# Kernel tuning notes

Hardware: AMD Instinct MI355X
Metric: run time of the kernel (lower is better)

Reference implementation:

```python
import jax, jax.numpy as jnp
import numpy as np

NUM_HEADS = 12
TOPK = 4


def setup_inputs() -> dict:
    key = jax.random.key(0)
    ks = jax.random.split(key, 5)
    B, N, C = 32, 577, 768
    s = 0.02
    return {
        "x": jax.random.normal(ks[0], (B, N, C), jnp.float32),
        "qkv_w": jax.random.normal(ks[1], (3 * C, C), jnp.float32) * s,
        "qkv_b": jax.random.normal(ks[2], (3 * C,), jnp.float32) * s,
        "proj_w": jax.random.normal(ks[3], (C, C), jnp.float32) * s,
        "proj_b": jax.random.normal(ks[4], (C,), jnp.float32) * s,
    }


def reference(x, qkv_w, qkv_b, proj_w, proj_b):
    B, N, C = x.shape
    H = NUM_HEADS
    D = C // H
    scale = D ** -0.5  # 0.125, matches original_attention.scale

    # qkv projection: (B,N,3C) -> (3,B,H,N,D)
    qkv = (x @ qkv_w.T + qkv_b).reshape(B, N, 3, H, D).transpose(2, 0, 3, 1, 4)
    q, k, v = qkv[0], qkv[1], qkv[2]

    # heuristic head routing: mean squared query energy per head
    scores = jnp.mean(q.astype(jnp.float32) ** 2, axis=(0, 2, 3))  # (H,)
    _, idx = jax.lax.top_k(scores, TOPK)
    idx = jnp.sort(idx)  # (topk,)

    q_sel = q[:, idx]  # (B,topk,N,D)
    k_sel = k[:, idx]
    v_sel = v[:, idx]

    attn = jax.nn.softmax(jnp.einsum('bhnd,bhmd->bhnm', q_sel, k_sel) * scale, axis=-1)
    y_sel = jnp.einsum('bhnm,bhmd->bhnd', attn, v_sel)  # (B,topk,N,D)

    # scatter selected heads back into full-size tensors (as in the torch module)
    y_full = jnp.zeros((B, H, N, D), x.dtype).at[:, idx].set(y_sel)
    x_out = y_full.transpose(0, 2, 1, 3).reshape(B, N, C) @ proj_w.T + proj_b

    attn_full = jnp.zeros((B, H, N, N), x.dtype).at[:, idx].set(attn)
    return x_out, attn_full
```

## Files before the change

kernel.cpp:

```cpp
#include <hip/hip_runtime.h>
#include <hip/hip_bf16.h>
#include <stdint.h>
#include <stddef.h>

#define B_ 32
#define N_ 577
#define C_ 768
#define H_ 12
#define D_ 64
#define M_ (B_*N_)
#define K3_ (3*C_)
#define NP_ 640
#define NN_ (N_*N_)

typedef __bf16 bf16x8_t __attribute__((ext_vector_type(8)));
typedef float f32x4 __attribute__((ext_vector_type(4)));
typedef unsigned short u16x8 __attribute__((ext_vector_type(8)));
typedef unsigned short u16x4 __attribute__((ext_vector_type(4)));

static __device__ __forceinline__ f32x4 mfma16(u16x8 a, u16x8 b, f32x4 c) {
  return __builtin_amdgcn_mfma_f32_16x16x32_bf16(
      __builtin_bit_cast(bf16x8_t, a), __builtin_bit_cast(bf16x8_t, b), c, 0, 0, 0);
}

static __device__ __forceinline__ unsigned short f2bf(float x) {
  unsigned int u = __builtin_bit_cast(unsigned int, x);
  u += 0x7fffu + ((u >> 16) & 1u);
  return (unsigned short)(u >> 16);
}

static __device__ __forceinline__ void glds16(const unsigned short* g, unsigned short* l) {
  __builtin_amdgcn_global_load_lds(
      (__attribute__((address_space(1))) void*)g,
      (__attribute__((address_space(3))) void*)l,
      16, 0, 0);
}

__global__ void k_cvt(const float* __restrict__ src, unsigned short* __restrict__ dst, int n4,
                      float* __restrict__ zeroptr) {
  if (zeroptr && blockIdx.x == 0 && threadIdx.x < 16) zeroptr[threadIdx.x] = 0.f;
  int stride = gridDim.x * blockDim.x;
  for (int i = blockIdx.x * blockDim.x + threadIdx.x; i < n4; i += stride) {
    float4 v = ((const float4*)src)[i];
    u16x4 o;
    o[0] = f2bf(v.x); o[1] = f2bf(v.y); o[2] = f2bf(v.z); o[3] = f2bf(v.w);
    *(u16x4*)(dst + (size_t)i * 4) = o;
  }
}

#define ZROWS_ 6
#define ZPER_ 146948
template<int MODE>
__global__ void k_gemm(const unsigned short* __restrict__ A,
                       const unsigned short* __restrict__ Bm,
                       const float* __restrict__ bias,
                       unsigned short* __restrict__ qb,
                       unsigned short* __restrict__ kb,
                       unsigned short* __restrict__ vb,
                       float* __restrict__ scores,
                       float* __restrict__ out,
                       int Mtot, int Ktot)
{
  __shared__ unsigned short As[128 * 32];
  __shared__ unsigned short Bs[128 * 32];
  const int tid = threadIdx.x;

  if (MODE == 0 && blockIdx.y < ZROWS_) {
    const int zblk = blockIdx.y * 145 + blockIdx.x;
    const size_t Z = (size_t)B_ * H_ * NN_;
    size_t s0 = (size_t)zblk * ZPER_;
    size_t len = ZPER_;
    if (s0 + len > Z) len = Z - s0;
    float* zo = out + s0;
    const float4 z4 = {0.f, 0.f, 0.f, 0.f};
    for (size_t t = tid * 4; t + 4 <= len; t += 4096)
      *(float4*)(zo + t) = z4;
    return;
  }

  const int bm = blockIdx.x;
  const int bn = (MODE == 0) ? (blockIdx.y - ZROWS_) : blockIdx.y;
  const int w = tid >> 6, l = tid & 63;
  const int wm = w >> 1, wn = w & 1;
  const int lr = l & 15, lg = l >> 4;
  const int lk = lg * 8;
  f32x4 acc[4][4] = {};
  const int rowA0 = bm * 128, rowB0 = bn * 128;
  const int le0 = w * 1024 + l * 8;
  const int kiters = Ktot >> 5;
  for (int kt = 0; kt < kiters; ++kt) {
    __syncthreads();
    #pragma unroll
    for (int c = 0; c < 2; ++c) {
      int lea = le0 + c * 512;
      int ra = lea >> 5, ka = lea & 31;
      glds16(A  + (size_t)(rowA0 + ra) * Ktot + kt * 32 + ka, As + (w * 2 + c) * 512);
      glds16(Bm + (size_t)(rowB0 + ra) * Ktot + kt * 32 + ka, Bs + (w * 2 + c) * 512);
    }
    __syncthreads();
    u16x8 af[4], bfr[4];
    #pragma unroll
    for (int i = 0; i < 4; ++i)
      af[i] = *(const u16x8*)(As + (wm * 64 + i * 16 + lr) * 32 + lk);
    #pragma unroll
    for (int j = 0; j < 4; ++j)
      bfr[j] = *(const u16x8*)(Bs + (wn * 64 + j * 16 + lr) * 32 + lk);
    #pragma unroll
    for (int i = 0; i < 4; ++i)
      #pragma unroll
      for (int j = 0; j < 4; ++j)
        acc[i][j] = mfma16(af[i], bfr[j], acc[i][j]);
  }

  const int rbase = lg * 4;
  if (MODE == 0) {
    const int n0 = rowB0 + wn * 64;
    const int t0 = n0 / C_;
    const int h0 = (n0 % C_) >> 6;
    unsigned short* dstbuf = (t0 == 0) ? qb : ((t0 == 1) ? kb : vb);
    float bs[4];
    #pragma unroll
    for (int j = 0; j < 4; ++j) bs[j] = bias[n0 + j * 16 + lr];
    float sq = 0.f;
    #pragma unroll
    for (int i = 0; i < 4; ++i) {
      const int mbase = rowA0 + wm * 64 + i * 16 + rbase;
      const int bb0 = mbase / N_;
      const int np0 = mbase - bb0 * N_;
      #pragma unroll
      for (int r = 0; r < 4; ++r) {
        const int mm = mbase + r;
        if (mm < Mtot) {
          int np = np0 + r, bb = bb0;
          if (np >= N_) { np -= N_; bb += 1; }
          unsigned short* drow = dstbuf + (((size_t)(bb * H_ + h0)) * N_ + np) * D_;
          #pragma unroll
          for (int j = 0; j < 4; ++j) {
            const float v = acc[i][j][r] + bs[j];
            if (t0 == 0) sq += v * v;
            drow[j * 16 + lr] = f2bf(v);
          }
        }
      }
    }
    if (t0 == 0) {
      #pragma unroll
      for (int s2 = 1; s2 < 64; s2 <<= 1) sq += __shfl_xor(sq, s2);
      if (l == 0) atomicAdd(scores + h0, sq);
    }
  } else {
    #pragma unroll
    for (int j = 0; j < 4; ++j) {
      const int n = rowB0 + wn * 64 + j * 16 + lr;
      const float bsj = bias[n];
      #pragma unroll
      for (int i = 0; i < 4; ++i) {
        const int mbase = rowA0 + wm * 64 + i * 16 + rbase;
        #pragma unroll
        for (int r = 0; r < 4; ++r) {
          const int mm = mbase + r;
          if (mm < Mtot) out[(size_t)mm * C_ + n] = acc[i][j][r] + bsj;
        }
      }
    }
  }
}

__global__ void k_topk(const float* __restrict__ scores, int* __restrict__ idxp) {
  if (threadIdx.x == 0 && blockIdx.x == 0) {
    float s[H_];
    bool used[H_];
    for (int i = 0; i < H_; ++i) { s[i] = scores[i]; used[i] = false; }
    int sel[4];
    for (int t = 0; t < 4; ++t) {
      int best = 0; float bv = -3.0e38f;
      for (int i = 0; i < H_; ++i)
        if (!used[i] && s[i] > bv) { bv = s[i]; best = i; }
      used[best] = true; sel[t] = best;
    }
    for (int a = 0; a < 4; ++a)
      for (int b = a + 1; b < 4; ++b)
        if (sel[b] < sel[a]) { int t = sel[a]; sel[a] = sel[b]; sel[b] = t; }
    for (int t = 0; t < 4; ++t) idxp[t] = sel[t];
  }
}

__global__ void k_gatherpw(const float* __restrict__ pw, const int* __restrict__ idxp,
                           unsigned short* __restrict__ pwsel) {
  int i = blockIdx.x * 256 + threadIdx.x;
  if (i >= C_ * 256) return;
  int c = i >> 8, j = i & 255;
  int h = idxp[j >> 6], d = j & 63;
  pwsel[i] = f2bf(pw[(size_t)c * C_ + h * 64 + d]);
}

__global__ void k_transv(const unsigned short* __restrict__ vb, unsigned short* __restrict__ vT,
                         const int* __restrict__ idxp) {
  __shared__ unsigned short t[64][72];
  const int bid = blockIdx.x;
  const int nt = bid % 10;
  const int p  = bid / 10;
  const int b  = p >> 2, hs = p & 3;
  const int h  = idxp[hs];
  const size_t bh_src = (size_t)(b * H_ + h);
  const size_t bh_dst = (size_t)(b * 4 + hs);
  const int n0 = nt * 64;
  const int tid = threadIdx.x;
  {
    const int r = tid >> 2, q4 = (tid & 3) * 16;
    const int n = n0 + r;
    u16x8 v0, v1;
    if (n < N_) {
      const unsigned short* src = vb + (bh_src * N_ + n) * D_ + q4;
      v0 = *(const u16x8*)(src);
      v1 = *(const u16x8*)(src + 8);
    } else {
      #pragma unroll
      for (int j = 0; j < 8; ++j) { v0[j] = 0; v1[j] = 0; }
    }
    *(u16x8*)&t[r][q4] = v0;
    *(u16x8*)&t[r][q4 + 8] = v1;
  }
  __syncthreads();
  {
    const int d = tid >> 2, nc = (tid & 3) * 16;
    u16x8 w0, w1;
    #pragma unroll
    for (int j = 0; j < 8; ++j) { w0[j] = t[nc + j][d]; w1[j] = t[nc + 8 + j][d]; }
    unsigned short* dst = vT + (bh_dst * D_ + d) * NP_ + n0 + nc;
    *(u16x8*)(dst) = w0;
    *(u16x8*)(dst + 8) = w1;
  }
}

__global__ void k_attn(const unsigned short* __restrict__ qb,
                       const unsigned short* __restrict__ kb,
                       const unsigned short* __restrict__ vT,
                       const int* __restrict__ idxp,
                       float* __restrict__ attn_out,
                       unsigned short* __restrict__ ysel)
{
  __shared__ unsigned short Plds[4][16][72];
  const int bid = blockIdx.x;

  const int qt = bid >> 7;
  const int pair = bid & 127;
  const int b  = pair >> 2;
  const int hs = pair & 3;
  const int h  = idxp[hs];
  const int tid = threadIdx.x;
  const int w = tid >> 6, l = tid & 63;
  const int lr = l & 15, lg = l >> 4, lk = lg * 8;
  const float sc2 = 0.125f * 1.44269504f;

  const size_t bh = (size_t)(b * H_ + h);
  const unsigned short* qbase = qb + bh * ((size_t)N_ * D_);
  const unsigned short* kbase = kb + bh * ((size_t)N_ * D_);
  const unsigned short* vbase = vT + (size_t)(b * 4 + hs) * ((size_t)D_ * NP_);
  float* aout = attn_out + bh * (size_t)NN_;

  const int qrow = qt * 64 + w * 16 + lr;
  const int qrc = (qrow < N_) ? qrow : (N_ - 1);
  u16x8 qf0 = *(const u16x8*)(qbase + (size_t)qrc * D_ + lk);
  u16x8 qf1 = *(const u16x8*)(qbase + (size_t)qrc * D_ + 32 + lk);

  float m2[4], lsum[4];
  #pragma unroll
  for (int r = 0; r < 4; ++r) { m2[r] = -1.0e30f; lsum[r] = 0.f; }

  for (int kt = 0; kt < 10; ++kt) {
    f32x4 s[4];
    bool vc[4];
    #pragma unroll
    for (int cg = 0; cg < 4; ++cg) {
      const int kc = kt * 64 + cg * 16 + lr;
      vc[cg] = (kc < N_);
      const int kcc = vc[cg] ? kc : (N_ - 1);
      const unsigned short* kp = kbase + (size_t)kcc * D_;
      u16x8 k0 = *(const u16x8*)(kp + lk);
      u16x8 k1 = *(const u16x8*)(kp + 32 + lk);
      f32x4 a = {0.f, 0.f, 0.f, 0.f};
      __builtin_amdgcn_s_setprio(1);
      a = mfma16(qf0, k0, a);
      a = mfma16(qf1, k1, a);
      __builtin_amdgcn_s_setprio(0);
      s[cg] = a;
    }
    #pragma unroll
    for (int r = 0; r < 4; ++r) {
      float tk[4];
      float mk = -1.0e30f;
      #pragma unroll
      for (int cg = 0; cg < 4; ++cg) {
        tk[cg] = vc[cg] ? s[cg][r] * sc2 : -1.0e30f;
        mk = fmaxf(mk, tk[cg]);
      }
      const float mn = fmaxf(m2[r], mk);
      float se = 0.f;
      #pragma unroll
      for (int cg = 0; cg < 4; ++cg)
        se += exp2f(tk[cg] - mn);
      lsum[r] = lsum[r] * exp2f(m2[r] - mn) + se;
      m2[r] = mn;
    }
  }
  #pragma unroll
  for (int x = 1; x < 16; x <<= 1) {
    #pragma unroll
    for (int r = 0; r < 4; ++r) {
      const float mo = __shfl_xor(m2[r], x);
      const float lo = __shfl_xor(lsum[r], x);
      const float mn = fmaxf(m2[r], mo);
      lsum[r] = lsum[r] * exp2f(m2[r] - mn) + lo * exp2f(mo - mn);
      m2[r] = mn;
    }
  }
  float off2[4];
  #pragma unroll
  for (int r = 0; r < 4; ++r) off2[r] = m2[r] + __log2f(lsum[r]);

  f32x4 y[4] = {};
  const int orow0 = qt * 64 + w * 16 + lg * 4;

  for (int kt = 0; kt < 10; ++kt) {
    f32x4 s[4];
    bool vc[4];
    #pragma unroll
    for (int cg = 0; cg < 4; ++cg) {
      const int kc = kt * 64 + cg * 16 + lr;
      vc[cg] = (kc < N_);
      const int kcc = vc[cg] ? kc : (N_ - 1);
      const unsigned short* kp = kbase + (size_t)kcc * D_;
      u16x8 k0 = *(const u16x8*)(kp + lk);
      u16x8 k1 = *(const u16x8*)(kp + 32 + lk);
      f32x4 a = {0.f, 0.f, 0.f, 0.f};
      __builtin_amdgcn_s_setprio(1);
      a = mfma16(qf0, k0, a);
      a = mfma16(qf1, k1, a);
      __builtin_amdgcn_s_setprio(0);
      s[cg] = a;
    }
    #pragma unroll
    for (int cg = 0; cg < 4; ++cg) {
      const int kc = kt * 64 + cg * 16 + lr;
      #pragma unroll
      for (int r = 0; r < 4; ++r) {
        float p = exp2f(__builtin_fmaf(s[cg][r], sc2, -off2[r]));
        p = vc[cg] ? p : 0.f;
        const int row = orow0 + r;
        if (vc[cg] && row < N_)
          aout[(size_t)row * N_ + kc] = p;
        Plds[w][lg * 4 + r][cg * 16 + lr] = f2bf(p);
      }
    }
    u16x8 pa0 = *(const u16x8*)&Plds[w][lr][lk];
    u16x8 pa1 = *(const u16x8*)&Plds[w][lr][32 + lk];
    #pragma unroll
    for (int cg2 = 0; cg2 < 4; ++cg2) {
      const unsigned short* vp = vbase + (size_t)(cg2 * 16 + lr) * NP_ + kt * 64;
      u16x8 v0 = *(const u16x8*)(vp + lk);
      u16x8 v1 = *(const u16x8*)(vp + 32 + lk);
      __builtin_amdgcn_s_setprio(1);
      y[cg2] = mfma16(pa0, v0, y[cg2]);
      y[cg2] = mfma16(pa1, v1, y[cg2]);
      __builtin_amdgcn_s_setprio(0);
    }
  }

  #pragma unroll
  for (int cg2 = 0; cg2 < 4; ++cg2)
    #pragma unroll
    for (int r = 0; r < 4; ++r) {
      const int row = orow0 + r;
      if (row < N_)
        ysel[((size_t)(b * N_ + row)) * 256 + hs * 64 + cg2 * 16 + lr] = f2bf(y[cg2][r]);
    }
}

extern "C" void kernel_launch(void* const* d_in, const int* in_sizes, int n_in,
                              void* d_out, int out_size, void* d_ws, size_t ws_size,
                              hipStream_t stream) {
  const float* x      = (const float*)d_in[0];
  const float* qkv_w  = (const float*)d_in[1];
  const float* qkv_b  = (const float*)d_in[2];
  const float* proj_w = (const float*)d_in[3];
  const float* proj_b = (const float*)d_in[4];

  float* xout = (float*)d_out;
  float* attn_out = (float*)d_out + (size_t)M_ * C_;

  char* ws = (char*)d_ws;
  size_t o = 0;
  unsigned short* xb    = (unsigned short*)(ws + o);
  unsigned short* vT    = (unsigned short*)(ws + o);
  o += 31457280;
  unsigned short* wqkvb = (unsigned short*)(ws + o); o += 3538944;
  unsigned short* qb    = (unsigned short*)(ws + o); o += 28360704;
  unsigned short* kb    = (unsigned short*)(ws + o); o += 28360704;
  unsigned short* vb    = (unsigned short*)(ws + o); o += 28360704;
  unsigned short* ysel  = (unsigned short*)(ws + o); o += 9453568;
  unsigned short* pwsel = (unsigned short*)(ws + o); o += 393216;
  float* scores         = (float*)(ws + o);
  int*   idxp           = (int*)(ws + o + 64);

  k_cvt<<<2048, 256, 0, stream>>>(x, xb, (M_ * C_) / 4, scores);
  k_cvt<<<1728, 256, 0, stream>>>(qkv_w, wqkvb, (K3_ * C_) / 4, nullptr);

  k_gemm<0><<<dim3(145, 18 + ZROWS_), 256, 0, stream>>>(xb, wqkvb, qkv_b,
                                               qb, kb, vb, scores, attn_out,
                                               M_, C_);

  k_topk<<<1, 64, 0, stream>>>(scores, idxp);
  k_gatherpw<<<768, 256, 0, stream>>>(proj_w, idxp, pwsel);
  k_transv<<<1280, 256, 0, stream>>>(vb, vT, idxp);

  k_attn<<<1280, 256, 0, stream>>>(qb, kb, vT, idxp, attn_out, ysel);

  k_gemm<1><<<dim3(145, 6), 256, 0, stream>>>(ysel, pwsel, proj_b,
                                              nullptr, nullptr, nullptr, nullptr, xout,
                                              M_, 256);
}
```

Before: 376.9 us.

## Merge small kernels and interleave zero-fill blocks with QKV GEMM tiles

Merges the two fp32-to-bf16 conversion launches into one kernel. Replaces the separate top-k, proj-weight gather and V-transpose kernels with a single prep kernel in which every block recomputes the top-4 head selection from the scores. The attention kernel also recomputes the selection itself, so the index buffer is no longer needed. In the QKV GEMM the attention-output zero-fill blocks are now spread across the grid's y rows instead of sitting at the front, so fill and GEMM work mix. The aim is fewer launches and better overlap, at the cost of redundant per-block top-k arithmetic.

```diff
diff --git a/kernel.cpp b/kernel.cpp
--- a/kernel.cpp
+++ b/kernel.cpp
@@ -36,11 +36,41 @@
       16, 0, 0);
 }
 
-__global__ void k_cvt(const float* __restrict__ src, unsigned short* __restrict__ dst, int n4,
-                      float* __restrict__ zeroptr) {
-  if (zeroptr && blockIdx.x == 0 && threadIdx.x < 16) zeroptr[threadIdx.x] = 0.f;
-  int stride = gridDim.x * blockDim.x;
-  for (int i = blockIdx.x * blockDim.x + threadIdx.x; i < n4; i += stride) {
+static __device__ __forceinline__ void top4sel(const float* __restrict__ scores, int* sel) {
+  float s[H_];
+  #pragma unroll
+  for (int i = 0; i < H_; ++i) s[i] = scores[i];
+  #pragma unroll
+  for (int t = 0; t < 4; ++t) {
+    int best = 0; float bv = s[0];
+    #pragma unroll
+    for (int i = 1; i < H_; ++i)
+      if (s[i] > bv) { bv = s[i]; best = i; }
+    sel[t] = best;
+    #pragma unroll
+    for (int i = 0; i < H_; ++i)
+      s[i] = (i == best) ? -3.0e38f : s[i];
+  }
+  #pragma unroll
+  for (int a = 0; a < 4; ++a)
+    #pragma unroll
+    for (int b2 = a + 1; b2 < 4; ++b2)
+      if (sel[b2] < sel[a]) { int t = sel[a]; sel[a] = sel[b2]; sel[b2] = t; }
+}
+
+__global__ void k_cvt2(const float* __restrict__ srcx, unsigned short* __restrict__ dstx, int n4x,
+                       const float* __restrict__ srcw, unsigned short* __restrict__ dstw, int n4w,
+                       float* __restrict__ zeroptr) {
+  if (blockIdx.x == 0 && threadIdx.x < 16) zeroptr[threadIdx.x] = 0.f;
+  const float* src; unsigned short* dst; int n4, i0, stride;
+  if (blockIdx.x < 2048) {
+    src = srcx; dst = dstx; n4 = n4x;
+    i0 = blockIdx.x * 256 + threadIdx.x; stride = 2048 * 256;
+  } else {
+    src = srcw; dst = dstw; n4 = n4w;
+    i0 = (blockIdx.x - 2048) * 256 + threadIdx.x; stride = 512 * 256;
+  }
+  for (int i = i0; i < n4; i += stride) {
     float4 v = ((const float4*)src)[i];
     u16x4 o;
     o[0] = f2bf(v.x); o[1] = f2bf(v.y); o[2] = f2bf(v.z); o[3] = f2bf(v.w);
@@ -48,7 +78,6 @@
   }
 }
 
-#define ZROWS_ 6
 #define ZPER_ 146948
 template<int MODE>
 __global__ void k_gemm(const unsigned short* __restrict__ A,
@@ -64,22 +93,28 @@
   __shared__ unsigned short As[128 * 32];
   __shared__ unsigned short Bs[128 * 32];
   const int tid = threadIdx.x;
-
-  if (MODE == 0 && blockIdx.y < ZROWS_) {
-    const int zblk = blockIdx.y * 145 + blockIdx.x;
-    const size_t Z = (size_t)B_ * H_ * NN_;
-    size_t s0 = (size_t)zblk * ZPER_;
-    size_t len = ZPER_;
-    if (s0 + len > Z) len = Z - s0;
-    float* zo = out + s0;
-    const float4 z4 = {0.f, 0.f, 0.f, 0.f};
-    for (size_t t = tid * 4; t + 4 <= len; t += 4096)
-      *(float4*)(zo + t) = z4;
-    return;
+  int bn;
+
+  if (MODE == 0) {
+    const int y = blockIdx.y;
+    if ((y & 3) == 0) {
+      const int zblk = (y >> 2) * 145 + blockIdx.x;
+      const size_t Z = (size_t)B_ * H_ * NN_;
+      size_t s0 = (size_t)zblk * ZPER_;
+      size_t len = ZPER_;
+      if (s0 + len > Z) len = Z - s0;
+      float* zo = out + s0;
+      const float4 z4 = {0.f, 0.f, 0.f, 0.f};
+      for (size_t t = tid * 4; t + 4 <= len; t += 4096)
+        *(float4*)(zo + t) = z4;
+      return;
+    }
+    bn = y - 1 - (y >> 2);
+  } else {
+    bn = blockIdx.y;
   }
 
   const int bm = blockIdx.x;
-  const int bn = (MODE == 0) ? (blockIdx.y - ZROWS_) : blockIdx.y;
   const int w = tid >> 6, l = tid & 63;
   const int wm = w >> 1, wn = w & 1;
   const int lr = l & 15, lg = l >> 4;
@@ -166,46 +201,30 @@
   }
 }
 
-__global__ void k_topk(const float* __restrict__ scores, int* __restrict__ idxp) {
-  if (threadIdx.x == 0 && blockIdx.x == 0) {
-    float s[H_];
-    bool used[H_];
-    for (int i = 0; i < H_; ++i) { s[i] = scores[i]; used[i] = false; }
-    int sel[4];
-    for (int t = 0; t < 4; ++t) {
-      int best = 0; float bv = -3.0e38f;
-      for (int i = 0; i < H_; ++i)
-        if (!used[i] && s[i] > bv) { bv = s[i]; best = i; }
-      used[best] = true; sel[t] = best;
-    }
-    for (int a = 0; a < 4; ++a)
-      for (int b = a + 1; b < 4; ++b)
-        if (sel[b] < sel[a]) { int t = sel[a]; sel[a] = sel[b]; sel[b] = t; }
-    for (int t = 0; t < 4; ++t) idxp[t] = sel[t];
-  }
-}
-
-__global__ void k_gatherpw(const float* __restrict__ pw, const int* __restrict__ idxp,
-                           unsigned short* __restrict__ pwsel) {
-  int i = blockIdx.x * 256 + threadIdx.x;
-  if (i >= C_ * 256) return;
-  int c = i >> 8, j = i & 255;
-  int h = idxp[j >> 6], d = j & 63;
-  pwsel[i] = f2bf(pw[(size_t)c * C_ + h * 64 + d]);
-}
-
-__global__ void k_transv(const unsigned short* __restrict__ vb, unsigned short* __restrict__ vT,
-                         const int* __restrict__ idxp) {
+__global__ void k_prep(const unsigned short* __restrict__ vb, unsigned short* __restrict__ vT,
+                       const float* __restrict__ scores,
+                       const float* __restrict__ pw, unsigned short* __restrict__ pwsel) {
+  int sel[4];
+  top4sel(scores, sel);
+  const int bid = blockIdx.x;
+  const int tid = threadIdx.x;
+
+  if (bid >= 1280) {
+    const int i = (bid - 1280) * 256 + tid;
+    const int c = i >> 8, j = i & 255;
+    const int h = sel[j >> 6], d = j & 63;
+    pwsel[i] = f2bf(pw[(size_t)c * C_ + h * 64 + d]);
+    return;
+  }
+
   __shared__ unsigned short t[64][72];
-  const int bid = blockIdx.x;
   const int nt = bid % 10;
   const int p  = bid / 10;
   const int b  = p >> 2, hs = p & 3;
-  const int h  = idxp[hs];
+  const int h  = sel[hs];
   const size_t bh_src = (size_t)(b * H_ + h);
   const size_t bh_dst = (size_t)(b * 4 + hs);
   const int n0 = nt * 64;
-  const int tid = threadIdx.x;
   {
     const int r = tid >> 2, q4 = (tid & 3) * 16;
     const int n = n0 + r;
@@ -236,18 +255,20 @@
 __global__ void k_attn(const unsigned short* __restrict__ qb,
                        const unsigned short* __restrict__ kb,
                        const unsigned short* __restrict__ vT,
-                       const int* __restrict__ idxp,
+                       const float* __restrict__ scores,
                        float* __restrict__ attn_out,
                        unsigned short* __restrict__ ysel)
 {
   __shared__ unsigned short Plds[4][16][72];
+  int sel[4];
+  top4sel(scores, sel);
   const int bid = blockIdx.x;
 
   const int qt = bid >> 7;
   const int pair = bid & 127;
   const int b  = pair >> 2;
   const int hs = pair & 3;
-  const int h  = idxp[hs];
+  const int h  = sel[hs];
   const int tid = threadIdx.x;
   const int w = tid >> 6, l = tid & 63;
   const int lr = l & 15, lg = l >> 4, lk = lg * 8;
@@ -401,20 +422,17 @@
   unsigned short* ysel  = (unsigned short*)(ws + o); o += 9453568;
   unsigned short* pwsel = (unsigned short*)(ws + o); o += 393216;
   float* scores         = (float*)(ws + o);
-  int*   idxp           = (int*)(ws + o + 64);
-
-  k_cvt<<<2048, 256, 0, stream>>>(x, xb, (M_ * C_) / 4, scores);
-  k_cvt<<<1728, 256, 0, stream>>>(qkv_w, wqkvb, (K3_ * C_) / 4, nullptr);
-
-  k_gemm<0><<<dim3(145, 18 + ZROWS_), 256, 0, stream>>>(xb, wqkvb, qkv_b,
+
+  k_cvt2<<<2560, 256, 0, stream>>>(x, xb, (M_ * C_) / 4,
+                                   qkv_w, wqkvb, (K3_ * C_) / 4, scores);
+
+  k_gemm<0><<<dim3(145, 24), 256, 0, stream>>>(xb, wqkvb, qkv_b,
                                                qb, kb, vb, scores, attn_out,
                                                M_, C_);
 
-  k_topk<<<1, 64, 0, stream>>>(scores, idxp);
-  k_gatherpw<<<768, 256, 0, stream>>>(proj_w, idxp, pwsel);
-  k_transv<<<1280, 256, 0, stream>>>(vb, vT, idxp);
-
-  k_attn<<<1280, 256, 0, stream>>>(qb, kb, vT, idxp, attn_out, ysel);
+  k_prep<<<2048, 256, 0, stream>>>(vb, vT, scores, proj_w, pwsel);
+
+  k_attn<<<1280, 256, 0, stream>>>(qb, kb, vT, scores, attn_out, ysel);
 
   k_gemm<1><<<dim3(145, 6), 256, 0, stream>>>(ysel, pwsel, proj_b,
                                               nullptr, nullptr, nullptr, nullptr, xout,
```

New measurement: 361.7 us. 4.0% less time.
